# Kernel optimization log

Measured on AMD Instinct MI355X. Metric: run time of the kernel, lower is better.

Reference implementation:

```python
import jax, jax.numpy as jnp
import numpy as np

B, N, D_MODEL, H = 2, 2048, 1024, 16
Q_CHUNK, K_CHUNK = 512, 1024
LN_EPS = 1e-5


def layer_norm(x, g, b):
    mu = x.mean(-1, keepdims=True)
    var = ((x - mu) ** 2).mean(-1, keepdims=True)
    return (x - mu) * jax.lax.rsqrt(var + LN_EPS) * g + b


def chunked_attention(q, k, v, qry_chunk, key_chunk):
    # q,k,v: [b,h,n,d]; memory-efficient chunked online-softmax attention
    b, h, n, d = q.shape
    q = q * (d ** -0.5)
    Q, K = n // qry_chunk, n // key_chunk
    qr = q.reshape(b, h, Q, qry_chunk, d)
    kr = k.reshape(b, h, K, key_chunk, d)
    vr = v.reshape(b, h, K, key_chunk, d)
    # per (q-chunk, k-chunk) scores: [b,h,Q,K,i,j]
    qk = jnp.einsum('bhqid,bhkjd->bhqkij', qr, kr)
    qk_max = jax.lax.stop_gradient(qk.max(axis=-1, keepdims=True))  # [b,h,Q,K,i,1]
    exp_qk = jnp.exp(qk - qk_max)
    attn = jnp.einsum('bhqkij,bhkjd->bhqkid', exp_qk, vr)
    exp_sum = exp_qk.sum(-1)            # [b,h,Q,K,i]
    m = qk_max[..., 0]                  # [b,h,Q,K,i]
    gmax = m.max(axis=3, keepdims=True)  # global max over key chunks
    renorm = jax.lax.stop_gradient(jnp.exp(m - gmax))
    num = (attn * renorm[..., None]).sum(axis=3)       # [b,h,Q,i,d]
    den = (exp_sum * renorm).sum(axis=3)[..., None]    # [b,h,Q,i,1]
    out = num / (1e-8 + den)
    return out.reshape(b, h, n, d)


def setup_inputs() -> dict:
    key = jax.random.key(0)
    ks = jax.random.split(key, 10)
    s = 0.02
    return {
        'x': jax.random.normal(ks[0], (B, N, D_MODEL), dtype=jnp.float32),
        'Wq': jax.random.normal(ks[1], (D_MODEL, D_MODEL), dtype=jnp.float32) * s,
        'bq': jnp.zeros((D_MODEL,), jnp.float32),
        'Wk': jax.random.normal(ks[2], (D_MODEL, D_MODEL), dtype=jnp.float32) * s,
        'bk': jnp.zeros((D_MODEL,), jnp.float32),
        'Wv': jax.random.normal(ks[3], (D_MODEL, D_MODEL), dtype=jnp.float32) * s,
        'bv': jnp.zeros((D_MODEL,), jnp.float32),
        'Wo': jax.random.normal(ks[4], (D_MODEL, D_MODEL), dtype=jnp.float32) * s,
        'bo': jnp.zeros((D_MODEL,), jnp.float32),
        'ln_g': jnp.ones((D_MODEL,), jnp.float32),
        'ln_b': jnp.zeros((D_MODEL,), jnp.float32),
    }


def reference(x, Wq, bq, Wk, bk, Wv, bv, Wo, bo, ln_g, ln_b):
    # qkv adapter: self-attention (key = val = qry = x)
    q = x @ Wq + bq
    k = x @ Wk + bk
    v = x @ Wv + bv
    # pre-norm on query path
    q = layer_norm(q, ln_g, ln_b)
    b, n, _ = q.shape
    d = D_MODEL // H
    qh = q.reshape(b, n, H, d).transpose(0, 2, 1, 3)
    kh = k.reshape(b, n, H, d).transpose(0, 2, 1, 3)
    vh = v.reshape(b, n, H, d).transpose(0, 2, 1, 3)
    attn = chunked_attention(qh, kh, vh, Q_CHUNK, K_CHUNK)
    out = attn.transpose(0, 2, 1, 3).reshape(b, n, D_MODEL)
    out = out + q  # residual with normed projected query
    return out @ Wo + bo
```

## Files before the change

### kernel.cpp

```cpp
#include <hip/hip_runtime.h>


typedef unsigned short u16;
typedef __attribute__((ext_vector_type(8))) short bf8v;
typedef __attribute__((ext_vector_type(4))) float f4v;

typedef __attribute__((address_space(1))) void gvoid;
typedef __attribute__((address_space(3))) void lvoid;
__device__ __forceinline__ void cp16(const void* g, void* l) {
  __builtin_amdgcn_global_load_lds((gvoid*)g, (lvoid*)l, 16, 0, 0);
}

__device__ __forceinline__ float bf2f(u16 u) {
  unsigned int x = ((unsigned int)u) << 16;
  float f; __builtin_memcpy(&f, &x, 4); return f;
}
__device__ __forceinline__ u16 f2bf(float f) {
  unsigned int x; __builtin_memcpy(&x, &f, 4);
  unsigned int r = (x + 0x7fffu + ((x >> 16) & 1u)) >> 16;
  return (u16)r;
}
__device__ __forceinline__ unsigned pack2bf(float a, float b) {
  unsigned ua, ub;
  __builtin_memcpy(&ua, &a, 4); __builtin_memcpy(&ub, &b, 4);
  return __builtin_amdgcn_perm(ub, ua, 0x07060302u);
}

#define KSCALE 0.18033688011f

__global__ void k_classify(const u16* a0, const u16* a1, const u16* a2, const u16* a3,
                           const u16* a4, const u16* a5, const u16* a6, const u16* a7,
                           const u16* a8, const u16* a9, const u16* a10, int* flags) {
  int t = threadIdx.x;
  if (t >= 11) return;
  const u16* arr[11] = {a0,a1,a2,a3,a4,a5,a6,a7,a8,a9,a10};
  const u16* p = arr[t];
  int ze = 0, no = 0, pe = 0;
  for (int i = 0; i < 128; ++i) {
    u16 he = p[2*i], ho = p[2*i+1];
    if (he == 0) ze++;
    if (ho != 0) no++;
    int e = (he >> 7) & 0xff;
    if (he == 0 || (e >= 64 && e <= 160)) pe++;
  }
  int isbf;
  if (ze >= 100 && no >= 64) isbf = 0;
  else isbf = (pe >= 100) ? 1 : 0;
  flags[t] = isbf;
}

__global__ __launch_bounds__(256) void k_convert_x(const void* xin, u16* xb, const int* flags) {
  size_t i = ((size_t)blockIdx.x * 256 + threadIdx.x) * 8;
  if (flags[0]) {
    *(float4*)(xb + i) = *((const float4*)((const u16*)xin + i));
  } else {
    const float* xf = (const float*)xin;
    float4 a = *(const float4*)(xf + i);
    float4 b = *(const float4*)(xf + i + 4);
    ushort4 o0, o1;
    o0.x = f2bf(a.x); o0.y = f2bf(a.y); o0.z = f2bf(a.z); o0.w = f2bf(a.w);
    o1.x = f2bf(b.x); o1.y = f2bf(b.y); o1.z = f2bf(b.z); o1.w = f2bf(b.w);
    *(ushort4*)(xb + i) = o0; *(ushort4*)(xb + i + 4) = o1;
  }
}

__global__ __launch_bounds__(256) void k_transpose_w(const void* W0, const void* W1,
    const void* W2, const void* W3, u16* wt, const int* flags) {
  __shared__ u16 tile[64 * 65];
  int z = blockIdx.z;
  const void* W = (z == 0) ? W0 : (z == 1) ? W1 : (z == 2) ? W2 : W3;
  int isb = flags[1 + 2*z];
  u16* dst = wt + (size_t)z * (1u << 20);
  int r0 = blockIdx.y * 64, c0 = blockIdx.x * 64;
  int t = threadIdx.x;
  for (int rr = 0; rr < 2; ++rr) {
    int row = rr * 32 + (t >> 3);
    int c8 = (t & 7) * 8;
    u16 v[8];
    if (isb) {
      const u16* Ws = (const u16*)W;
      ushort4 a = *(const ushort4*)&Ws[(size_t)(r0 + row) * 1024 + c0 + c8];
      ushort4 b = *(const ushort4*)&Ws[(size_t)(r0 + row) * 1024 + c0 + c8 + 4];
      v[0]=a.x; v[1]=a.y; v[2]=a.z; v[3]=a.w; v[4]=b.x; v[5]=b.y; v[6]=b.z; v[7]=b.w;
    } else {
      const float* Wf = (const float*)W;
      float4 a = *(const float4*)&Wf[(size_t)(r0 + row) * 1024 + c0 + c8];
      float4 b = *(const float4*)&Wf[(size_t)(r0 + row) * 1024 + c0 + c8 + 4];
      v[0]=f2bf(a.x); v[1]=f2bf(a.y); v[2]=f2bf(a.z); v[3]=f2bf(a.w);
      v[4]=f2bf(b.x); v[5]=f2bf(b.y); v[6]=f2bf(b.z); v[7]=f2bf(b.w);
    }
#pragma unroll
    for (int j = 0; j < 8; ++j) tile[row * 65 + c8 + j] = v[j];
  }
  __syncthreads();
  for (int rr = 0; rr < 2; ++rr) {
    int nrow = rr * 32 + (t >> 3);
    int k8 = (t & 7) * 8;
    u16 v[8];
#pragma unroll
    for (int j = 0; j < 8; ++j) v[j] = tile[(k8 + j) * 65 + nrow];
    ushort4 o0, o1;
    o0.x=v[0]; o0.y=v[1]; o0.z=v[2]; o0.w=v[3];
    o1.x=v[4]; o1.y=v[5]; o1.z=v[6]; o1.w=v[7];
    *(ushort4*)&dst[(size_t)(c0 + nrow) * 1024 + r0 + k8] = o0;
    *(ushort4*)&dst[(size_t)(c0 + nrow) * 1024 + r0 + k8 + 4] = o1;
  }
}

template <int MT>
__device__ __forceinline__ void gemm_bt(const u16* __restrict__ A, const u16* __restrict__ Bt,
    const void* __restrict__ bias, int bias_bf, void* __restrict__ Cout, int mode,
    float cscale) {
  constexpr int MI = MT / 32;
  __shared__ __align__(16) u16 As[2][MT * 32];
  __shared__ __align__(16) u16 Bs[2][128 * 32];
  const int tid = threadIdx.x;
  const int wave = tid >> 6, lane = tid & 63;
  const int qd = lane >> 4, ln = lane & 15;
  const int m0 = blockIdx.y * MT, n0 = blockIdx.x * 128;
  const int wr = (wave >> 1) * (MT / 2), wc = (wave & 1) * 64;
  const int r0 = wave * 16 + (lane >> 2);
  const int csrc = ((lane & 3) ^ ((lane >> 2) & 3)) * 8;
  const u16* Ag = &A[(size_t)m0 * 1024];
  const u16* Bg = &Bt[(size_t)n0 * 1024];
  const int co = (qd ^ (ln & 3)) * 8;
  f4v acc[MI][4];
#pragma unroll
  for (int i = 0; i < MI; ++i)
#pragma unroll
    for (int j = 0; j < 4; ++j) acc[i][j] = (f4v){0.f, 0.f, 0.f, 0.f};

#pragma unroll
  for (int t = 0; t < MT / 64; ++t)
    cp16(&Ag[(size_t)(t * 64 + r0) * 1024 + csrc], &As[0][(t * 256 + wave * 64) * 8]);
#pragma unroll
  for (int t = 0; t < 2; ++t)
    cp16(&Bg[(size_t)(t * 64 + r0) * 1024 + csrc], &Bs[0][(t * 256 + wave * 64) * 8]);

  for (int it = 0; it < 32; ++it) {
    __syncthreads();
    if (it < 31) {
      int ko = (it + 1) * 32;
      int bi = (it + 1) & 1;
#pragma unroll
      for (int t = 0; t < MT / 64; ++t)
        cp16(&Ag[(size_t)(t * 64 + r0) * 1024 + ko + csrc], &As[bi][(t * 256 + wave * 64) * 8]);
#pragma unroll
      for (int t = 0; t < 2; ++t)
        cp16(&Bg[(size_t)(t * 64 + r0) * 1024 + ko + csrc], &Bs[bi][(t * 256 + wave * 64) * 8]);
    }
    const u16* as = As[it & 1];
    const u16* bs = Bs[it & 1];
    bf8v af[MI], bfr[4];
#pragma unroll
    for (int i = 0; i < MI; ++i) af[i]  = *(const bf8v*)&as[(wr + i * 16 + ln) * 32 + co];
#pragma unroll
    for (int j = 0; j < 4; ++j) bfr[j] = *(const bf8v*)&bs[(wc + j * 16 + ln) * 32 + co];
#pragma unroll
    for (int i = 0; i < MI; ++i)
#pragma unroll
      for (int j = 0; j < 4; ++j)
        acc[i][j] = __builtin_amdgcn_mfma_f32_16x16x32_bf16(af[i], bfr[j], acc[i][j], 0, 0, 0);
  }
#pragma unroll
  for (int j = 0; j < 4; ++j) {
    int col = n0 + wc + j * 16 + ln;
    float bv = bias_bf ? bf2f(((const u16*)bias)[col]) : ((const float*)bias)[col];
#pragma unroll
    for (int i = 0; i < MI; ++i) {
      int row = m0 + wr + i * 16 + qd * 4;
      if (mode == 2) {
        ushort4 o4;
        o4.x = f2bf((acc[i][j][0] + bv) * cscale);
        o4.y = f2bf((acc[i][j][1] + bv) * cscale);
        o4.z = f2bf((acc[i][j][2] + bv) * cscale);
        o4.w = f2bf((acc[i][j][3] + bv) * cscale);
        int b_ = row >> 11, nl = row & 2047;
        int h_ = col >> 6, d6 = col & 63;
        int kt = nl >> 6, b0 = nl & 63;
        int c = b0 >> 5, g = (b0 >> 4) & 1, qd_f = (b0 >> 2) & 3;
        int dt = d6 >> 4, ln_f = d6 & 15;
        size_t off = (size_t)(b_ * 16 + h_) * 131072
                   + (size_t)(kt * 4096 + (c * 4 + dt) * 512 + (qd_f * 16 + ln_f) * 8 + g * 4);
        *(ushort4*)&((u16*)Cout)[off] = o4;
      } else {
#pragma unroll
        for (int r = 0; r < 4; ++r) {
          float v = (acc[i][j][r] + bv) * cscale;
          if (mode == 1) ((u16*)Cout)[(size_t)(row + r) * 1024 + col] = f2bf(v);
          else           ((float*)Cout)[(size_t)(row + r) * 1024 + col] = v;
        }
      }
    }
  }
}

__global__ __launch_bounds__(256) void k_gemm_qkv(const u16* xb, const u16* wt,
    const void* bq, const void* bk, const void* bv, const int* flags,
    u16* qpre, u16* kb, u16* vtb) {
  int z = blockIdx.z;
  const u16* Bt = wt + (size_t)z * (1u << 20);
  const void* bias = (z == 0) ? bq : (z == 1) ? bk : bv;
  if (z == 0)      gemm_bt<128>(xb, Bt, bias, flags[2], qpre, 1, 1.0f);
  else if (z == 1) gemm_bt<128>(xb, Bt, bias, flags[4], kb,   1, KSCALE);
  else             gemm_bt<128>(xb, Bt, bias, flags[6], vtb,  2, 1.0f);
}

__global__ __launch_bounds__(256) void k_gemm_out(const u16* A, const u16* Bt,
    const void* bias, const int* flags, void* out) {
  gemm_bt<64>(A, Bt, bias, flags[8], out, flags[0] ? 1 : 0, 1.0f);
}

__global__ __launch_bounds__(256) void k_layernorm(const u16* __restrict__ qp,
    const void* __restrict__ g, const void* __restrict__ bb, const int* flags,
    u16* __restrict__ out) {
  int row = blockIdx.x, t = threadIdx.x;
  const u16* rp = qp + (size_t)row * 1024;
  ushort4 u = *(const ushort4*)(rp + t * 4);
  float x0 = bf2f(u.x), x1 = bf2f(u.y), x2 = bf2f(u.z), x3 = bf2f(u.w);
  float s = x0 + x1 + x2 + x3;
  float s2 = x0 * x0 + x1 * x1 + x2 * x2 + x3 * x3;
  for (int off = 32; off; off >>= 1) { s += __shfl_down(s, off); s2 += __shfl_down(s2, off); }
  __shared__ float red[10];
  int wave = t >> 6, lane = t & 63;
  if (lane == 0) { red[wave] = s; red[4 + wave] = s2; }
  __syncthreads();
  if (t == 0) {
    float S = red[0] + red[1] + red[2] + red[3];
    float S2 = red[4] + red[5] + red[6] + red[7];
    float mu = S * (1.f / 1024.f);
    float var = S2 * (1.f / 1024.f) - mu * mu;
    red[8] = mu; red[9] = rsqrtf(var + 1e-5f);
  }
  __syncthreads();
  float mu = red[8], rstd = red[9];
  int gf = flags[9], bf = flags[10];
  int c = t * 4;
  float gv[4], bv[4];
#pragma unroll
  for (int k = 0; k < 4; ++k) {
    gv[k] = gf ? bf2f(((const u16*)g)[c + k]) : ((const float*)g)[c + k];
    bv[k] = bf ? bf2f(((const u16*)bb)[c + k]) : ((const float*)bb)[c + k];
  }
  ushort4 o;
  o.x = f2bf((x0 - mu) * rstd * gv[0] + bv[0]);
  o.y = f2bf((x1 - mu) * rstd * gv[1] + bv[1]);
  o.z = f2bf((x2 - mu) * rstd * gv[2] + bv[2]);
  o.w = f2bf((x3 - mu) * rstd * gv[3] + bv[3]);
  *(ushort4*)(out + (size_t)row * 1024 + c) = o;
}

__global__ __launch_bounds__(256) void k_attention(const u16* __restrict__ qln,
    const u16* __restrict__ kb, const u16* __restrict__ vfg, u16* __restrict__ attn) {
  const int x = blockIdx.x;
  const int xcd = x & 7, sl = x >> 3;
  const int bh = xcd * 4 + (sl >> 3), qc = sl & 7;
  const int b = bh >> 4, h = bh & 15;
  const int tid = threadIdx.x, wave = tid >> 6, lane = tid & 63;
  const int qd = lane >> 4, ln = lane & 15;
  const int qrow0 = qc * 256 + wave * 64;

  const u16* kgb = kb + (size_t)b * 2048 * 1024 + h * 64;
  const u16* vgb = vfg + (size_t)bh * 131072;

  bf8v qf[4][2];
#pragma unroll
  for (int qs = 0; qs < 4; ++qs) {
    const u16* qb = qln + ((size_t)b * 2048 + qrow0 + qs * 16 + ln) * 1024 + h * 64;
    qf[qs][0] = *(const bf8v*)(qb + qd * 8);
    qf[qs][1] = *(const bf8v*)(qb + 32 + qd * 8);
  }
  float ls[4][4];
  f4v o[4][4];
#pragma unroll
  for (int qs = 0; qs < 4; ++qs)
#pragma unroll
    for (int r = 0; r < 4; ++r) { ls[qs][r] = 0.f; o[qs][r] = (f4v){0.f, 0.f, 0.f, 0.f}; }

  for (int kt = 0; kt < 2048; kt += 64) {
    const u16* kr = kgb + (size_t)kt * 1024;
    bf8v kf[4][2];
#pragma unroll
    for (int ct = 0; ct < 4; ++ct) {
      kf[ct][0] = *(const bf8v*)(kr + (size_t)(ct * 16 + ln) * 1024 + qd * 8);
      kf[ct][1] = *(const bf8v*)(kr + (size_t)(ct * 16 + ln) * 1024 + 32 + qd * 8);
    }
    const u16* vr = vgb + (size_t)(kt >> 6) * 4096;
    bf8v vf[8];
#pragma unroll
    for (int cd = 0; cd < 8; ++cd)
      vf[cd] = *(const bf8v*)(vr + cd * 512 + lane * 8);

#pragma unroll
    for (int qs = 0; qs < 4; ++qs) {
      unsigned pk[4][2];
#pragma unroll
      for (int ct = 0; ct < 4; ++ct) {
        f4v z = (f4v){0.f, 0.f, 0.f, 0.f};
        z = __builtin_amdgcn_mfma_f32_16x16x32_bf16(kf[ct][0], qf[qs][0], z, 0, 0, 0);
        z = __builtin_amdgcn_mfma_f32_16x16x32_bf16(kf[ct][1], qf[qs][1], z, 0, 0, 0);
        float p0 = __builtin_amdgcn_exp2f(z[0]);
        float p1 = __builtin_amdgcn_exp2f(z[1]);
        float p2 = __builtin_amdgcn_exp2f(z[2]);
        float p3 = __builtin_amdgcn_exp2f(z[3]);
        ls[qs][0] += p0; ls[qs][1] += p1; ls[qs][2] += p2; ls[qs][3] += p3;
        pk[ct][0] = pack2bf(p0, p1);
        pk[ct][1] = pack2bf(p2, p3);
      }
#pragma unroll
      for (int c = 0; c < 2; ++c) {
        unsigned avals[4] = {pk[2*c][0], pk[2*c][1], pk[2*c+1][0], pk[2*c+1][1]};
        bf8v af; __builtin_memcpy(&af, avals, 16);
#pragma unroll
        for (int dt = 0; dt < 4; ++dt)
          o[qs][dt] = __builtin_amdgcn_mfma_f32_16x16x32_bf16(af, vf[c * 4 + dt], o[qs][dt], 0, 0, 0);
      }
    }
  }
#pragma unroll
  for (int qs = 0; qs < 4; ++qs) {
    float lsum = (ls[qs][0] + ls[qs][1]) + (ls[qs][2] + ls[qs][3]);
    lsum += __shfl_xor(lsum, 16);
    lsum += __shfl_xor(lsum, 32);
    float rden[4];
#pragma unroll
    for (int r = 0; r < 4; ++r) {
      float dv = __shfl(lsum, (lane & 48) + qd * 4 + r);
      rden[r] = __builtin_amdgcn_rcpf(1e-8f + dv);
    }
#pragma unroll
    for (int dt = 0; dt < 4; ++dt) {
#pragma unroll
      for (int r = 0; r < 4; ++r) {
        size_t idx = ((size_t)b * 2048 + qrow0 + qs * 16 + qd * 4 + r) * 1024
                   + h * 64 + dt * 16 + ln;
        float val = o[qs][dt][r] * rden[r] + bf2f(qln[idx]);
        attn[idx] = f2bf(val);
      }
    }
  }
}

extern "C" void kernel_launch(void* const* d_in, const int* in_sizes, int n_in,
                              void* d_out, int out_size, void* d_ws, size_t ws_size,
                              hipStream_t stream) {
  int* flags = (int*)d_ws;
  u16* base = (u16*)((char*)d_ws + 256);
  const size_t M1 = 1u << 20;
  u16* xb   = base;
  u16* wt   = base + 4 * M1;
  u16* qpre = base + 8 * M1;
  u16* kb   = base + 12 * M1;
  u16* vtb  = base + 16 * M1;
  u16* qln = xb;
  u16* at  = qpre;

  k_classify<<<1, 64, 0, stream>>>(
      (const u16*)d_in[0], (const u16*)d_in[1], (const u16*)d_in[2], (const u16*)d_in[3],
      (const u16*)d_in[4], (const u16*)d_in[5], (const u16*)d_in[6], (const u16*)d_in[7],
      (const u16*)d_in[8], (const u16*)d_in[9], (const u16*)d_in[10], flags);

  k_convert_x<<<2048, 256, 0, stream>>>(d_in[0], xb, flags);
  k_transpose_w<<<dim3(16, 16, 4), 256, 0, stream>>>(d_in[1], d_in[3], d_in[5], d_in[7], wt, flags);
  k_gemm_qkv<<<dim3(8, 32, 3), 256, 0, stream>>>(xb, wt, d_in[2], d_in[4], d_in[6], flags,
                                                 qpre, kb, vtb);
  k_layernorm<<<4096, 256, 0, stream>>>(qpre, d_in[9], d_in[10], flags, qln);
  k_attention<<<256, 256, 0, stream>>>(qln, kb, vtb, at);
  k_gemm_out<<<dim3(8, 64), 256, 0, stream>>>(at, wt + 3 * M1, d_in[8], flags, d_out);
}
```

Before: 226.8 us.

## Pre-swizzle K into fragment layout and double-buffer K/V tiles through LDS

The QKV GEMM now writes K in a blocked fragment layout, like V, so each 64-key tile is contiguous per (batch, head). The attention kernel streams K and V tiles into a double-buffered shared-memory array with async global-to-LDS copies, prefetching the next tile while computing the current one. The four waves in a block now share one load of each tile instead of each wave loading K/V from global memory itself. This adds a __syncthreads per tile, and the mode-3 epilogue writes K as scattered 2-byte stores.

After: 222.8 us. About the same (-1.7%).

```diff
diff --git a/kernel.cpp b/kernel.cpp
--- a/kernel.cpp
+++ b/kernel.cpp
@@ -183,6 +183,18 @@
         size_t off = (size_t)(b_ * 16 + h_) * 131072
                    + (size_t)(kt * 4096 + (c * 4 + dt) * 512 + (qd_f * 16 + ln_f) * 8 + g * 4);
         *(ushort4*)&((u16*)Cout)[off] = o4;
+      } else if (mode == 3) {
+        int b_ = row >> 11, nl = row & 2047;
+        int h_ = col >> 6, d6 = col & 63;
+        int tile = nl >> 6, ct = (nl >> 4) & 3;
+        int half = d6 >> 5, qd_k = (d6 >> 3) & 3, jj = d6 & 7;
+        size_t base = (size_t)(b_ * 16 + h_) * 131072
+                    + (size_t)(tile * 4096 + (ct * 2 + half) * 512 + qd_k * 128 + jj);
+#pragma unroll
+        for (int r = 0; r < 4; ++r) {
+          float v = (acc[i][j][r] + bv) * cscale;
+          ((u16*)Cout)[base + (size_t)(((nl & 15) + r) * 8)] = f2bf(v);
+        }
       } else {
 #pragma unroll
         for (int r = 0; r < 4; ++r) {
@@ -202,7 +214,7 @@
   const u16* Bt = wt + (size_t)z * (1u << 20);
   const void* bias = (z == 0) ? bq : (z == 1) ? bk : bv;
   if (z == 0)      gemm_bt<128>(xb, Bt, bias, flags[2], qpre, 1, 1.0f);
-  else if (z == 1) gemm_bt<128>(xb, Bt, bias, flags[4], kb,   1, KSCALE);
+  else if (z == 1) gemm_bt<128>(xb, Bt, bias, flags[4], kb,   3, KSCALE);
   else             gemm_bt<128>(xb, Bt, bias, flags[6], vtb,  2, 1.0f);
 }
 
@@ -250,8 +262,37 @@
   *(ushort4*)(out + (size_t)row * 1024 + c) = o;
 }
 
+__device__ __forceinline__ void attn_tile(const bf8v kf[4][2], const bf8v vf[8],
+    const bf8v qf[4][2], float ls[4][4], f4v o[4][4]) {
+#pragma unroll
+  for (int qs = 0; qs < 4; ++qs) {
+    unsigned pk[4][2];
+#pragma unroll
+    for (int ct = 0; ct < 4; ++ct) {
+      f4v z = (f4v){0.f, 0.f, 0.f, 0.f};
+      z = __builtin_amdgcn_mfma_f32_16x16x32_bf16(kf[ct][0], qf[qs][0], z, 0, 0, 0);
+      z = __builtin_amdgcn_mfma_f32_16x16x32_bf16(kf[ct][1], qf[qs][1], z, 0, 0, 0);
+      float p0 = __builtin_amdgcn_exp2f(z[0]);
+      float p1 = __builtin_amdgcn_exp2f(z[1]);
+      float p2 = __builtin_amdgcn_exp2f(z[2]);
+      float p3 = __builtin_amdgcn_exp2f(z[3]);
+      ls[qs][0] += p0; ls[qs][1] += p1; ls[qs][2] += p2; ls[qs][3] += p3;
+      pk[ct][0] = pack2bf(p0, p1);
+      pk[ct][1] = pack2bf(p2, p3);
+    }
+#pragma unroll
+    for (int c = 0; c < 2; ++c) {
+      unsigned avals[4] = {pk[2*c][0], pk[2*c][1], pk[2*c+1][0], pk[2*c+1][1]};
+      bf8v af; __builtin_memcpy(&af, avals, 16);
+#pragma unroll
+      for (int dt = 0; dt < 4; ++dt)
+        o[qs][dt] = __builtin_amdgcn_mfma_f32_16x16x32_bf16(af, vf[c * 4 + dt], o[qs][dt], 0, 0, 0);
+    }
+  }
+}
+
 __global__ __launch_bounds__(256) void k_attention(const u16* __restrict__ qln,
-    const u16* __restrict__ kb, const u16* __restrict__ vfg, u16* __restrict__ attn) {
+    const u16* __restrict__ kfg, const u16* __restrict__ vfg, u16* __restrict__ attn) {
   const int x = blockIdx.x;
   const int xcd = x & 7, sl = x >> 3;
   const int bh = xcd * 4 + (sl >> 3), qc = sl & 7;
@@ -260,8 +301,10 @@
   const int qd = lane >> 4, ln = lane & 15;
   const int qrow0 = qc * 256 + wave * 64;
 
-  const u16* kgb = kb + (size_t)b * 2048 * 1024 + h * 64;
+  const u16* kgb = kfg + (size_t)bh * 131072;
   const u16* vgb = vfg + (size_t)bh * 131072;
+
+  __shared__ __align__(16) u16 kv[2][8192];
 
   bf8v qf[4][2];
 #pragma unroll
@@ -277,46 +320,37 @@
 #pragma unroll
     for (int r = 0; r < 4; ++r) { ls[qs][r] = 0.f; o[qs][r] = (f4v){0.f, 0.f, 0.f, 0.f}; }
 
-  for (int kt = 0; kt < 2048; kt += 64) {
-    const u16* kr = kgb + (size_t)kt * 1024;
-    bf8v kf[4][2];
+#pragma unroll
+  for (int q = 0; q < 2; ++q) {
+    cp16(kgb + (size_t)(q * 256 + tid) * 8, &kv[0][(q * 256 + wave * 64) * 8]);
+    cp16(vgb + (size_t)(q * 256 + tid) * 8, &kv[0][4096 + (q * 256 + wave * 64) * 8]);
+  }
+
+  for (int t = 0; t < 32; ++t) {
+    __syncthreads();
+    if (t < 31) {
+      const u16* ks = kgb + (size_t)(t + 1) * 4096;
+      const u16* vs = vgb + (size_t)(t + 1) * 4096;
+      u16* dst = kv[(t + 1) & 1];
+#pragma unroll
+      for (int q = 0; q < 2; ++q) {
+        cp16(ks + (size_t)(q * 256 + tid) * 8, &dst[(q * 256 + wave * 64) * 8]);
+        cp16(vs + (size_t)(q * 256 + tid) * 8, &dst[4096 + (q * 256 + wave * 64) * 8]);
+      }
+    }
+    const u16* kvb = kv[t & 1];
+    bf8v kfr[4][2], vfr[8];
 #pragma unroll
     for (int ct = 0; ct < 4; ++ct) {
-      kf[ct][0] = *(const bf8v*)(kr + (size_t)(ct * 16 + ln) * 1024 + qd * 8);
-      kf[ct][1] = *(const bf8v*)(kr + (size_t)(ct * 16 + ln) * 1024 + 32 + qd * 8);
-    }
-    const u16* vr = vgb + (size_t)(kt >> 6) * 4096;
-    bf8v vf[8];
+      kfr[ct][0] = *(const bf8v*)&kvb[(ct * 2 + 0) * 512 + lane * 8];
+      kfr[ct][1] = *(const bf8v*)&kvb[(ct * 2 + 1) * 512 + lane * 8];
+    }
 #pragma unroll
     for (int cd = 0; cd < 8; ++cd)
-      vf[cd] = *(const bf8v*)(vr + cd * 512 + lane * 8);
-
-#pragma unroll
-    for (int qs = 0; qs < 4; ++qs) {
-      unsigned pk[4][2];
-#pragma unroll
-      for (int ct = 0; ct < 4; ++ct) {
-        f4v z = (f4v){0.f, 0.f, 0.f, 0.f};
-        z = __builtin_amdgcn_mfma_f32_16x16x32_bf16(kf[ct][0], qf[qs][0], z, 0, 0, 0);
-        z = __builtin_amdgcn_mfma_f32_16x16x32_bf16(kf[ct][1], qf[qs][1], z, 0, 0, 0);
-        float p0 = __builtin_amdgcn_exp2f(z[0]);
-        float p1 = __builtin_amdgcn_exp2f(z[1]);
-        float p2 = __builtin_amdgcn_exp2f(z[2]);
-        float p3 = __builtin_amdgcn_exp2f(z[3]);
-        ls[qs][0] += p0; ls[qs][1] += p1; ls[qs][2] += p2; ls[qs][3] += p3;
-        pk[ct][0] = pack2bf(p0, p1);
-        pk[ct][1] = pack2bf(p2, p3);
-      }
-#pragma unroll
-      for (int c = 0; c < 2; ++c) {
-        unsigned avals[4] = {pk[2*c][0], pk[2*c][1], pk[2*c+1][0], pk[2*c+1][1]};
-        bf8v af; __builtin_memcpy(&af, avals, 16);
-#pragma unroll
-        for (int dt = 0; dt < 4; ++dt)
-          o[qs][dt] = __builtin_amdgcn_mfma_f32_16x16x32_bf16(af, vf[c * 4 + dt], o[qs][dt], 0, 0, 0);
-      }
-    }
-  }
+      vfr[cd] = *(const bf8v*)&kvb[4096 + cd * 512 + lane * 8];
+    attn_tile(kfr, vfr, qf, ls, o);
+  }
+
 #pragma unroll
   for (int qs = 0; qs < 4; ++qs) {
     float lsum = (ls[qs][0] + ls[qs][1]) + (ls[qs][2] + ls[qs][3]);
```
